# Optimization experiments

Hardware: AMD Instinct MI355X
Metric: run time of the kernel (lower is better)

## Reference

```python
import jax, jax.numpy as jnp
import numpy as np

B, T, C, H = 4, 2048, 1024, 16
HS = C // H  # head_size = 64
EPS = 1e-5


def setup_inputs() -> dict:
    key = jax.random.key(0)
    ks = jax.random.split(key, 16)
    s = 0.02
    inp = {
        "x": jax.random.normal(ks[0], (B, T, C), jnp.float32),
        # custom LayerNorm buffers (gamma=ones, beta=zeros in source)
        "ln1_g": jnp.ones((C,), jnp.float32),
        "ln1_b": jnp.zeros((C,), jnp.float32),
        "ln2_g": jnp.ones((C,), jnp.float32),
        "ln2_b": jnp.zeros((C,), jnp.float32),
        # per-head Q/K/V linears, stacked over heads: [H, C, HS]
        "Wq": jax.random.normal(ks[1], (H, C, HS), jnp.float32) * s,
        "bq": jax.random.normal(ks[2], (H, HS), jnp.float32) * s,
        "Wk": jax.random.normal(ks[3], (H, C, HS), jnp.float32) * s,
        "bk": jax.random.normal(ks[4], (H, HS), jnp.float32) * s,
        "Wv": jax.random.normal(ks[5], (H, C, HS), jnp.float32) * s,
        "bv": jax.random.normal(ks[6], (H, HS), jnp.float32) * s,
        # output projection [C, C]
        "Wo": jax.random.normal(ks[7], (C, C), jnp.float32) * s,
        "bo": jax.random.normal(ks[8], (C,), jnp.float32) * s,
        # FFN: C -> 4C -> C
        "W1": jax.random.normal(ks[9], (C, 4 * C), jnp.float32) * s,
        "b1": jax.random.normal(ks[10], (4 * C,), jnp.float32) * s,
        "W2": jax.random.normal(ks[11], (4 * C, C), jnp.float32) * s,
        "b2": jax.random.normal(ks[12], (C,), jnp.float32) * s,
    }
    return inp


def _layernorm_time_axis(x, g, b):
    # Faithful to source: normalizes over axis=1 (time), unbiased variance (ddof=1).
    m = jnp.mean(x, axis=1, keepdims=True)
    v = jnp.var(x, axis=1, keepdims=True, ddof=1)
    return g * (x - m) / jnp.sqrt(v + EPS) + b


def reference(x, ln1_g, ln1_b, ln2_g, ln2_b, Wq, bq, Wk, bk, Wv, bv, Wo, bo, W1, b1, W2, b2):
    Bc, Tc, Cc = x.shape
    h = _layernorm_time_axis(x, ln1_g, ln1_b)
    # per-head projections: [B, H, T, HS]
    q = jnp.einsum('btc,hcd->bhtd', h, Wq) + bq[None, :, None, :]
    k = jnp.einsum('btc,hcd->bhtd', h, Wk) + bk[None, :, None, :]
    v = jnp.einsum('btc,hcd->bhtd', h, Wv) + bv[None, :, None, :]
    # scores scaled by C**-0.5 (full embed dim, as in source)
    wei = jnp.einsum('bhtd,bhsd->bhts', q, k) * (Cc ** -0.5)
    causal = jnp.tril(jnp.ones((Tc, Tc), bool))
    wei = jnp.where(causal[None, None], wei, -jnp.inf)
    wei = jax.nn.softmax(wei, axis=-1)
    att = jnp.einsum('bhts,bhsd->bhtd', wei, v)
    # concat heads -> [B, T, C], then projection
    att = att.transpose(0, 2, 1, 3).reshape(Bc, Tc, Cc)
    x = x + att @ Wo + bo
    # FFN on ln2
    h2 = _layernorm_time_axis(x, ln2_g, ln2_b)
    ff = jax.nn.relu(h2 @ W1 + b1) @ W2 + b2
    return x + ff
```

## Files before the change

kernel.cpp:

```cpp
#include <hip/hip_runtime.h>

#define B_   4
#define T_   2048
#define C_   1024
#define H_   16
#define HS_  64
#define BT_  (B_*T_)
#define EPS_ 1e-5f

typedef unsigned short u16;
typedef unsigned int   u32;
typedef __attribute__((ext_vector_type(8))) __bf16 bf16x8;
typedef __attribute__((ext_vector_type(4))) float  f32x4;
typedef __attribute__((ext_vector_type(8))) u16    u16x8;
typedef __attribute__((ext_vector_type(4))) u16    u16x4;
typedef __attribute__((ext_vector_type(4))) u32    u32x4;

__device__ __forceinline__ u16 f2bf(float f) {
  unsigned x = __builtin_bit_cast(unsigned, f);
  x += 0x7fffu + ((x >> 16) & 1u);
  return (u16)(x >> 16);
}
__device__ __forceinline__ float bf2f(u16 v) {
  return __builtin_bit_cast(float, (u32)v << 16);
}

__device__ __forceinline__ float fast_exp2(float x) {
  float y;
  asm("v_exp_f32 %0, %1" : "=v"(y) : "v"(x));
  return y;
}
__device__ __forceinline__ float fast_rcp(float x) {
  float y;
  asm("v_rcp_f32 %0, %1" : "=v"(y) : "v"(x));
  return y;
}

#define GLD_LDS16(src, dst) \
  __builtin_amdgcn_global_load_lds((__attribute__((address_space(1))) void*)(src), \
                                   (__attribute__((address_space(3))) void*)(dst), 16, 0, 0)

__global__ __launch_bounds__(256) void ln_partial_bf(const u16* __restrict__ x,
                                                     float* __restrict__ ps,
                                                     float* __restrict__ psq) {
  int col = blockIdx.x * 256 + threadIdx.x;
  int b = col >> 10, c = col & (C_ - 1);
  int t0 = blockIdx.y * (T_ / 16);
  const u16* p = x + (size_t)b * T_ * C_ + (size_t)t0 * C_ + c;
  float s = 0.f, sq = 0.f;
  #pragma unroll 4
  for (int i = 0; i < T_ / 16; ++i) { float v = bf2f(p[(size_t)i * C_]); s += v; sq += v * v; }
  ps [blockIdx.y * (B_ * C_) + col] = s;
  psq[blockIdx.y * (B_ * C_) + col] = sq;
}

__global__ __launch_bounds__(256) void ln_final(const float* __restrict__ ps,
                                                const float* __restrict__ psq,
                                                float* __restrict__ mean,
                                                float* __restrict__ rstd) {
  int col = blockIdx.x * 256 + threadIdx.x;
  float s = 0.f, sq = 0.f;
  #pragma unroll
  for (int i = 0; i < 16; ++i) { s += ps[i * (B_ * C_) + col]; sq += psq[i * (B_ * C_) + col]; }
  float m = s * (1.f / T_);
  float var = (sq - (float)T_ * m * m) * (1.f / (T_ - 1));
  mean[col] = m;
  rstd[col] = rsqrtf(var + EPS_);
}

__global__ __launch_bounds__(256) void ln_norm(const float* __restrict__ x,
                                               const float* __restrict__ mean,
                                               const float* __restrict__ rstd,
                                               const float* __restrict__ gam,
                                               const float* __restrict__ bet,
                                               u16* __restrict__ out) {
  size_t i = ((size_t)blockIdx.x * 256 + threadIdx.x) * 4;
  int c  = (int)(i & (C_ - 1));
  int b  = (int)(i >> 21);
  int bc = (b << 10) + c;
  float4 v = *(const float4*)(x + i);
  float vv[4] = {v.x, v.y, v.z, v.w};
  u16x4 o;
  #pragma unroll
  for (int j = 0; j < 4; ++j)
    o[j] = f2bf(gam[c + j] * (vv[j] - mean[bc + j]) * rstd[bc + j] + bet[c + j]);
  *(u16x4*)(out + i) = o;
}

__global__ __launch_bounds__(256) void ln_norm_bf(const u16* __restrict__ x,
                                                  const float* __restrict__ mean,
                                                  const float* __restrict__ rstd,
                                                  const float* __restrict__ gam,
                                                  const float* __restrict__ bet,
                                                  u16* __restrict__ out) {
  size_t i = ((size_t)blockIdx.x * 256 + threadIdx.x) * 4;
  int c  = (int)(i & (C_ - 1));
  int b  = (int)(i >> 21);
  int bc = (b << 10) + c;
  u16x4 v = *(const u16x4*)(x + i);
  u16x4 o;
  #pragma unroll
  for (int j = 0; j < 4; ++j)
    o[j] = f2bf(gam[c + j] * (bf2f(v[j]) - mean[bc + j]) * rstd[bc + j] + bet[c + j]);
  *(u16x4*)(out + i) = o;
}

__global__ __launch_bounds__(256) void pack_all(
    const float* __restrict__ Wq, const float* __restrict__ Wk,
    const float* __restrict__ Wv, const float* __restrict__ Wo,
    const float* __restrict__ W1, const float* __restrict__ W2,
    const float* __restrict__ bq, const float* __restrict__ bk,
    const float* __restrict__ bv, const float* __restrict__ x,
    u16* __restrict__ wqkvT, u16* __restrict__ woT,
    u16* __restrict__ w1T,   u16* __restrict__ w2T,
    float* __restrict__ bqkv,
    float* __restrict__ ps,  float* __restrict__ psq) {
  __shared__ float tile[32][33];
  const int bid = blockIdx.x;
  const int tid = threadIdx.x;

  if (bid >= 12300) {
    const int rel = bid - 12300;
    const int bx = rel & 15, by = rel >> 4;
    int col = bx * 256 + tid;
    int b = col >> 10, c = col & (C_ - 1);
    int t0 = by * (T_ / 16);
    const float* p = x + (size_t)b * T_ * C_ + (size_t)t0 * C_ + c;
    float s = 0.f, sq = 0.f;
    #pragma unroll 4
    for (int i = 0; i < T_ / 16; ++i) { float v = p[(size_t)i * C_]; s += v; sq += v * v; }
    ps [by * (B_ * C_) + col] = s;
    psq[by * (B_ * C_) + col] = sq;
    return;
  }
  if (bid >= 12288) {
    int i = (bid - 12288) * 256 + tid;
    float v = (i < 1024) ? bq[i] : (i < 2048 ? bk[i - 1024] : bv[i - 2048]);
    bqkv[i] = v;
    return;
  }

  const float* I; u16* Ou; int cols_in, ld_out, bx, by;
  if (bid < 3072) {
    const int z = bid >> 6, t6 = bid & 63;
    bx = t6 & 1; by = t6 >> 1;
    const int wsel = z >> 4, head = z & 15;
    I  = (wsel == 0 ? Wq : (wsel == 1 ? Wk : Wv)) + (size_t)head * (C_ * 64);
    Ou = wqkvT + (size_t)wsel * 1024 * 1024 + (size_t)head * 64 * 1024;
    cols_in = 64; ld_out = 1024;
  } else if (bid < 4096) {
    const int rel = bid - 3072;
    bx = rel & 31; by = rel >> 5;
    I = Wo; Ou = woT; cols_in = 1024; ld_out = 1024;
  } else if (bid < 8192) {
    const int rel = bid - 4096;
    bx = rel & 127; by = rel >> 7;
    I = W1; Ou = w1T; cols_in = 4096; ld_out = 1024;
  } else {
    const int rel = bid - 8192;
    bx = rel & 31; by = rel >> 5;
    I = W2; Ou = w2T; cols_in = 1024; ld_out = 4096;
  }

  const int r0 = by << 5, c0 = bx << 5;
  const int tx = tid & 31, ty = tid >> 5;
  #pragma unroll
  for (int rr = 0; rr < 32; rr += 8)
    tile[ty + rr][tx] = I[(size_t)(r0 + ty + rr) * cols_in + c0 + tx];
  __syncthreads();
  #pragma unroll
  for (int rr = 0; rr < 32; rr += 8)
    Ou[(size_t)(c0 + ty + rr) * ld_out + r0 + tx] = f2bf(tile[tx][ty + rr]);
}

__global__ __launch_bounds__(256) void v_transpose(const u16* __restrict__ qkv,
                                                   u16* __restrict__ Vt) {
  __shared__ u16 tile[32][33];
  int bh = blockIdx.z; int b = bh >> 4, h = bh & 15;
  int t0 = blockIdx.x << 5, hs0 = blockIdx.y << 5;
  int tx = threadIdx.x & 31, ty = threadIdx.x >> 5;
  const u16* src = qkv + (size_t)(b * T_ + t0) * 3072 + 2048 + h * 64 + hs0;
  #pragma unroll
  for (int rr = 0; rr < 32; rr += 8)
    tile[ty + rr][tx] = src[(size_t)(ty + rr) * 3072 + tx];
  __syncthreads();
  u16* dst = Vt + ((size_t)bh * 64 + hs0) * T_ + t0;
  #pragma unroll
  for (int rr = 0; rr < 32; rr += 8)
    dst[(size_t)(ty + rr) * T_ + tx] = tile[tx][ty + rr];
}

template<int BN, int RELU, int QSCALE>
__global__ __launch_bounds__(256, 2)
void gemm_128t(const u16* __restrict__ A,
               const u16* __restrict__ Bt,
               const float* __restrict__ bias,
               u16* __restrict__ outp,
               int M, int N, int K) {
  constexpr int BK  = 32;
  constexpr int CHA = 2;
  constexpr int CHB = BN / 64;
  constexpr int NF  = BN / 32;

  __shared__ u16 sA[3][128 * BK];
  __shared__ u16 sB[3][BN * BK];

  const int tid = threadIdx.x;
  const int wave = tid >> 6, lane = tid & 63;
  const int g = lane >> 4, r16 = lane & 15;

  const int nbx = N / BN;
  const int nwg = gridDim.x;
  const int bid = blockIdx.x;
  const int swz = ((bid & 7) * (nwg >> 3)) + (bid >> 3);
  const int bx = swz % nbx, by = swz / nbx;
  const int row0 = by << 7, col0 = bx * BN;

  const u16* aS[CHA];
  const u16* bS[CHB];
  #pragma unroll
  for (int j = 0; j < CHA; ++j) {
    const int ci = tid + 256 * j, row = ci >> 2, cc = ci & 3;
    aS[j] = A + (size_t)(row0 + row) * K + ((cc ^ ((row >> 1) & 3)) * 8);
  }
  #pragma unroll
  for (int j = 0; j < CHB; ++j) {
    const int ci = tid + 256 * j, row = ci >> 2, cc = ci & 3;
    bS[j] = Bt + (size_t)(col0 + row) * K + ((cc ^ ((row >> 1) & 3)) * 8);
  }
  const int ldsOff = wave * 512;

  auto stage = [&](int t, int buf) {
    const int ko = t * BK;
    #pragma unroll
    for (int j = 0; j < CHA; ++j)
      GLD_LDS16(aS[j] + ko, &sA[buf][ldsOff + j * 2048]);
    #pragma unroll
    for (int j = 0; j < CHB; ++j)
      GLD_LDS16(bS[j] + ko, &sB[buf][ldsOff + j * 2048]);
  };

  auto wait_stage1 = [&]() {
    if constexpr (CHB == 4) asm volatile("s_waitcnt vmcnt(6)" ::: "memory");
    else                    asm volatile("s_waitcnt vmcnt(5)" ::: "memory");
  };

  const int wrow = (wave >> 1) * 64;
  const int wcol = (wave & 1) * (BN >> 1);
  f32x4 acc[4][NF] = {};

  const int NT = K / BK;

  stage(0, 0); stage(1, 1);
  wait_stage1();
  __builtin_amdgcn_s_barrier();
  __builtin_amdgcn_sched_barrier(0);

  for (int t = 0; t < NT; ++t) {
    const u16* As = sA[t % 3];
    const u16* Bs = sB[t % 3];
    bf16x8 af[4], bf[NF];
    #pragma unroll
    for (int m = 0; m < 4; ++m) {
      const int lr = wrow + m * 16 + r16;
      af[m] = *(const bf16x8*)&As[lr * 32 + ((g ^ ((lr >> 1) & 3)) * 8)];
    }
    #pragma unroll
    for (int n = 0; n < NF; ++n) {
      const int lr = wcol + n * 16 + r16;
      bf[n] = *(const bf16x8*)&Bs[lr * 32 + ((g ^ ((lr >> 1) & 3)) * 8)];
    }
    if (t + 2 < NT) stage(t + 2, (t + 2) % 3);

    __builtin_amdgcn_s_setprio(1);
    #pragma unroll
    for (int m = 0; m < 4; ++m)
      #pragma unroll
      for (int n = 0; n < NF; ++n)
        acc[m][n] = __builtin_amdgcn_mfma_f32_16x16x32_bf16(af[m], bf[n], acc[m][n], 0, 0, 0);
    __builtin_amdgcn_s_setprio(0);

    if (t + 1 < NT) {
      if (t + 2 < NT) wait_stage1();
      else            asm volatile("s_waitcnt vmcnt(0)" ::: "memory");
      __builtin_amdgcn_s_barrier();
      __builtin_amdgcn_sched_barrier(0);
    }
  }

  #pragma unroll
  for (int m = 0; m < 4; ++m) {
    #pragma unroll
    for (int n = 0; n < NF; ++n) {
      const int col = col0 + wcol + n * 16 + r16;
      const float bv = bias[col];
      const float sc = (QSCALE && col < 1024) ? 0.04508422003f : 1.f;
      const int rowb = row0 + wrow + m * 16 + g * 4;
      #pragma unroll
      for (int r = 0; r < 4; ++r) {
        float v = acc[m][n][r] + bv;
        if (RELU) v = fmaxf(v, 0.f);
        if (QSCALE) v *= sc;
        outp[(size_t)(rowb + r) * N + col] = f2bf(v);
      }
    }
  }
}

template<int RELU, int RAW, int QSCALE>
__global__ __launch_bounds__(512, 2)
void gemm_256(const u16* __restrict__ A,
              const u16* __restrict__ Bt,
              const float* __restrict__ bias,
              const u16* __restrict__ resb,
              void* __restrict__ outp,
              void* __restrict__ outp_b,
              int M, int N, int K) {
  constexpr int BK = 32;
  __shared__ u16 sA[4][256 * BK];
  __shared__ u16 sB[4][256 * BK];

  const int tid = threadIdx.x;
  const int wave = tid >> 6, lane = tid & 63;
  const int g = lane >> 4, r16 = lane & 15;

  const int nbx = N >> 8;
  const int nwg = gridDim.x;
  const int bid = blockIdx.x;
  const int swz = ((bid & 7) * (nwg >> 3)) + (bid >> 3);
  const int bx = swz % nbx, by = swz / nbx;
  const int row0 = by << 8, col0 = bx << 8;

  const int kspan = RAW ? (K >> 1) : K;
  const int kbase = RAW ? ((int)blockIdx.y * kspan) : 0;

  const u16* aS[2];
  const u16* bS[2];
  #pragma unroll
  for (int j = 0; j < 2; ++j) {
    const int ci = tid + 512 * j, row = ci >> 2, cc = ci & 3;
    aS[j] = A  + (size_t)(row0 + row) * K + ((cc ^ ((row >> 1) & 3)) * 8) + kbase;
    bS[j] = Bt + (size_t)(col0 + row) * K + ((cc ^ ((row >> 1) & 3)) * 8) + kbase;
  }
  const int ldsOff = wave * 512;

  auto stage = [&](int t, int buf) {
    const int ko = t * BK;
    #pragma unroll
    for (int j = 0; j < 2; ++j)
      GLD_LDS16(aS[j] + ko, &sA[buf][ldsOff + j * 4096]);
    #pragma unroll
    for (int j = 0; j < 2; ++j)
      GLD_LDS16(bS[j] + ko, &sB[buf][ldsOff + j * 4096]);
  };

  const int wrow = (wave >> 2) * 128;
  const int wcol = (wave & 3) * 64;
  f32x4 acc[8][4] = {};

  const int NT = kspan / BK;

  stage(0, 0); stage(1, 1);
  asm volatile("s_waitcnt vmcnt(4)" ::: "memory");
  __builtin_amdgcn_s_barrier();
  __builtin_amdgcn_sched_barrier(0);

  for (int t = 0; t < NT; ++t) {
    const u16* As = sA[t & 3];
    const u16* Bs = sB[t & 3];
    bf16x8 af[8], bf[4];
    #pragma unroll
    for (int m = 0; m < 8; ++m) {
      const int lr = wrow + m * 16 + r16;
      af[m] = *(const bf16x8*)&As[lr * 32 + ((g ^ ((lr >> 1) & 3)) * 8)];
    }
    #pragma unroll
    for (int n = 0; n < 4; ++n) {
      const int lr = wcol + n * 16 + r16;
      bf[n] = *(const bf16x8*)&Bs[lr * 32 + ((g ^ ((lr >> 1) & 3)) * 8)];
    }
    if (t + 2 < NT) stage(t + 2, (t + 2) & 3);

    __builtin_amdgcn_s_setprio(1);
    #pragma unroll
    for (int m = 0; m < 8; ++m)
      #pragma unroll
      for (int n = 0; n < 4; ++n)
        acc[m][n] = __builtin_amdgcn_mfma_f32_16x16x32_bf16(af[m], bf[n], acc[m][n], 0, 0, 0);
    __builtin_amdgcn_s_setprio(0);

    if (t + 1 < NT) {
      if (t + 2 < NT) asm volatile("s_waitcnt vmcnt(4)" ::: "memory");
      else            asm volatile("s_waitcnt vmcnt(0)" ::: "memory");
      __builtin_amdgcn_s_barrier();
      __builtin_amdgcn_sched_barrier(0);
    }
  }

  if constexpr (RAW) {
    if (blockIdx.y) {
      float* po = (float*)outp_b;
      #pragma unroll
      for (int m = 0; m < 8; ++m) {
        #pragma unroll
        for (int n = 0; n < 4; ++n) {
          const int col = col0 + wcol + n * 16 + r16;
          const float bv = bias[col];
          const int rowb = row0 + wrow + m * 16 + g * 4;
          #pragma unroll
          for (int r = 0; r < 4; ++r) {
            const size_t idx = (size_t)(rowb + r) * N + col;
            po[idx] = acc[m][n][r] + bv + bf2f(resb[idx]);
          }
        }
      }
    } else {
      u16* po = (u16*)outp;
      #pragma unroll
      for (int m = 0; m < 8; ++m) {
        #pragma unroll
        for (int n = 0; n < 4; ++n) {
          const int col = col0 + wcol + n * 16 + r16;
          const int rowb = row0 + wrow + m * 16 + g * 4;
          #pragma unroll
          for (int r = 0; r < 4; ++r)
            po[(size_t)(rowb + r) * N + col] = f2bf(acc[m][n][r]);
        }
      }
    }
  } else {
    u16* po = (u16*)outp;
    #pragma unroll
    for (int m = 0; m < 8; ++m) {
      #pragma unroll
      for (int n = 0; n < 4; ++n) {
        const int col = col0 + wcol + n * 16 + r16;
        const float bv = bias[col];
        const float sc = (QSCALE && col < 1024) ? 0.04508422003f : 1.f;
        const int rowb = row0 + wrow + m * 16 + g * 4;
        #pragma unroll
        for (int r = 0; r < 4; ++r) {
          float v = acc[m][n][r] + bv;
          if (RELU) v = fmaxf(v, 0.f);
          if (QSCALE) v *= sc;
          po[(size_t)(rowb + r) * N + col] = f2bf(v);
        }
      }
    }
  }
}

__global__ __launch_bounds__(256) void ffn2_reduce(const u16* __restrict__ pA,
                                                   float* __restrict__ out) {
  size_t i = ((size_t)blockIdx.x * 256 + threadIdx.x) * 4;
  u16x4 a = *(const u16x4*)(pA + i);
  float4 o = *(const float4*)(out + i);
  float4 v;
  v.x = o.x + bf2f(a[0]);
  v.y = o.y + bf2f(a[1]);
  v.z = o.z + bf2f(a[2]);
  v.w = o.w + bf2f(a[3]);
  *(float4*)(out + i) = v;
}

template<int BM, int BN, int THREADS, int OUT_F32, int RELU, int RES>
__global__ __launch_bounds__(THREADS, 3)
void gemm_pipe(const u16* __restrict__ A,
               const u16* __restrict__ Bt,
               const float* __restrict__ bias,
               const float* __restrict__ res,
               void* __restrict__ outp,
               int M, int N, int K) {
  constexpr int BK  = 32;
  constexpr int CHA = (BM * 4) / THREADS;
  constexpr int CHB = (BN * 4) / THREADS;
  constexpr int CH  = CHA + CHB;

  __shared__ u16 sA[3][BM * BK];
  __shared__ u16 sB[3][BN * BK];

  const int tid = threadIdx.x;
  const int wave = tid >> 6, lane = tid & 63;
  const int g = lane >> 4, r16 = lane & 15;

  const int nbx = N / BN;
  const int nwg = gridDim.x;
  const int bid = blockIdx.x;
  const int swz = ((bid & 7) * (nwg >> 3)) + (bid >> 3);
  const int bx = swz % nbx, by = swz / nbx;
  const int row0 = by * BM, col0 = bx * BN;

  const u16* aS[CHA];
  const u16* bS[CHB];
  #pragma unroll
  for (int j = 0; j < CHA; ++j) {
    const int ci = tid + THREADS * j, row = ci >> 2, cc = ci & 3;
    aS[j] = A + (size_t)(row0 + row) * K + ((cc ^ ((row >> 1) & 3)) * 8);
  }
  #pragma unroll
  for (int j = 0; j < CHB; ++j) {
    const int ci = tid + THREADS * j, row = ci >> 2, cc = ci & 3;
    bS[j] = Bt + (size_t)(col0 + row) * K + ((cc ^ ((row >> 1) & 3)) * 8);
  }
  const int ldsOff = wave * 512;

  auto stage = [&](int t, int buf) {
    const int ko = t * BK;
    #pragma unroll
    for (int j = 0; j < CHA; ++j)
      GLD_LDS16(aS[j] + ko, &sA[buf][ldsOff + j * (THREADS * 8)]);
    #pragma unroll
    for (int j = 0; j < CHB; ++j)
      GLD_LDS16(bS[j] + ko, &sB[buf][ldsOff + j * (THREADS * 8)]);
  };

  const int wrow = (wave >> 1) * 64;
  const int wcol = (wave & 1) * 64;
  f32x4 acc[4][4] = {};

  const int NT = K / BK;

  stage(0, 0); stage(1, 1);
  if constexpr (CH == 3) asm volatile("s_waitcnt vmcnt(3)" ::: "memory");
  else                   asm volatile("s_waitcnt vmcnt(4)" ::: "memory");
  __builtin_amdgcn_s_barrier();
  __builtin_amdgcn_sched_barrier(0);

  for (int t = 0; t < NT; ++t) {
    if (t + 2 < NT) stage(t + 2, (t + 2) % 3);
    const u16* As = sA[t % 3];
    const u16* Bs = sB[t % 3];
    bf16x8 af[4], bf[4];
    #pragma unroll
    for (int m = 0; m < 4; ++m) {
      const int lr = wrow + m * 16 + r16;
      af[m] = *(const bf16x8*)&As[lr * 32 + ((g ^ ((lr >> 1) & 3)) * 8)];
    }
    #pragma unroll
    for (int n = 0; n < 4; ++n) {
      const int lr = wcol + n * 16 + r16;
      bf[n] = *(const bf16x8*)&Bs[lr * 32 + ((g ^ ((lr >> 1) & 3)) * 8)];
    }
    __builtin_amdgcn_s_setprio(1);
    #pragma unroll
    for (int m = 0; m < 4; ++m)
      #pragma unroll
      for (int n = 0; n < 4; ++n)
        acc[m][n] = __builtin_amdgcn_mfma_f32_16x16x32_bf16(af[m], bf[n], acc[m][n], 0, 0, 0);
    __builtin_amdgcn_s_setprio(0);

    if (t + 1 < NT) {
      if (t + 2 < NT) {
        if constexpr (CH == 3) asm volatile("s_waitcnt vmcnt(3)" ::: "memory");
        else                   asm volatile("s_waitcnt vmcnt(4)" ::: "memory");
      } else {
        asm volatile("s_waitcnt vmcnt(0)" ::: "memory");
      }
      __builtin_amdgcn_s_barrier();
      __builtin_amdgcn_sched_barrier(0);
    }
  }

  #pragma unroll
  for (int m = 0; m < 4; ++m) {
    #pragma unroll
    for (int n = 0; n < 4; ++n) {
      const int col = col0 + wcol + n * 16 + r16;
      const float bv = bias[col];
      const int rowb = row0 + wrow + m * 16 + g * 4;
      #pragma unroll
      for (int r = 0; r < 4; ++r) {
        const size_t idx = (size_t)(rowb + r) * N + col;
        float v = acc[m][n][r] + bv;
        if (RES)  v += res[idx];
        if (RELU) v = fmaxf(v, 0.f);
        if (OUT_F32) ((float*)outp)[idx] = v;
        else         ((u16*)outp)[idx]   = f2bf(v);
      }
    }
  }
}

__global__ __launch_bounds__(256, 2) void attn_fwd(const u16* __restrict__ qkv,
                                                   const u16* __restrict__ Vt,
                                                   u16* __restrict__ O) {
  __shared__ u16 sK[2][64 * 64];
  __shared__ u16 sV[2][64 * 64];

  const int orig = blockIdx.x;
  const int work = ((orig & 7) << 6) + (orig >> 3);
  const int i = work & 7;
  const int h = (work >> 3) & 15;
  const int b = work >> 7;
  const int qA = i << 7, qB = (15 - i) << 7;
  const int nA = 2 * i + 2, nB = 32 - 2 * i;

  const int tid = threadIdx.x, wave = tid >> 6, lane = tid & 63;
  const int g = lane >> 4, r16 = lane & 15;

  const size_t base = (size_t)b * T_ * 3072 + h * 64;
  const u16* Qp = qkv + base;
  const u16* Kp = qkv + base + 1024;
  const u16* VtP = Vt + (size_t)(b * 16 + h) * 64 * T_;

  const int rowL = lane >> 3;
  const int colL = 8 * ((lane & 7) ^ rowL);
  const u16* kSrc = Kp  + (size_t)(wave * 16 + rowL) * 3072 + colL;
  const u16* vSrc = VtP + (size_t)(wave * 16 + rowL) * T_   + colL;
  u16* kDst0 = &sK[0][(wave * 16 + 0) * 64];
  u16* kDst8 = &sK[0][(wave * 16 + 8) * 64];
  u16* vDst0 = &sV[0][(wave * 16 + 0) * 64];
  u16* vDst8 = &sV[0][(wave * 16 + 8) * 64];

  const int ck0 = (( 0 + g * 16) ^ ((r16 & 7) << 4)) >> 1;
  const int ck1 = ((64 + g * 16) ^ ((r16 & 7) << 4)) >> 1;

  bf16x8 qfA[2][2], qfB[2][2];
  #pragma unroll
  for (int qp = 0; qp < 2; ++qp)
    #pragma unroll
    for (int kc = 0; kc < 2; ++kc) {
      qfA[qp][kc] = *(const bf16x8*)(Qp + (size_t)(qA + wave * 32 + qp * 16 + r16) * 3072 + kc * 32 + g * 8);
      qfB[qp][kc] = *(const bf16x8*)(Qp + (size_t)(qB + wave * 32 + qp * 16 + r16) * 3072 + kc * 32 + g * 8);
    }

  f32x4 accA[2][4] = {}, accB[2][4] = {};
  f32x4 lA[2] = {}, lB[2] = {};
  int qaA[2], qaB[2];
  #pragma unroll
  for (int qp = 0; qp < 2; ++qp) {
    qaA[qp] = qA + wave * 32 + qp * 16 + r16;
    qaB[qp] = qB + wave * 32 + qp * 16 + r16;
  }

  const u32 one2 = 0x3F803F80u;
  const u32x4 onesv = {one2, one2, one2, one2};
  const bf16x8 ONES = __builtin_bit_cast(bf16x8, onesv);

  int sbuf = 0;
  auto stageAdv = [&]() {
    const int o = sbuf * 4096;
    GLD_LDS16(kSrc,            kDst0 + o);
    GLD_LDS16(kSrc + 8 * 3072, kDst8 + o);
    GLD_LDS16(vSrc,            vDst0 + o);
    GLD_LDS16(vSrc + 8 * T_,   vDst8 + o);
    kSrc += 64 * 3072;
    vSrc += 64;
    sbuf ^= 1;
  };

  auto qkt = [&](const bf16x8* kf0, const bf16x8* kf1, const bf16x8* qf, f32x4* s) {
    __builtin_amdgcn_s_setprio(1);
    #pragma unroll
    for (int ni = 0; ni < 4; ++ni) {
      f32x4 t = {};
      t = __builtin_amdgcn_mfma_f32_16x16x32_bf16(kf0[ni], qf[0], t, 0, 0, 0);
      t = __builtin_amdgcn_mfma_f32_16x16x32_bf16(kf1[ni], qf[1], t, 0, 0, 0);
      s[ni] = t;
    }
    __builtin_amdgcn_s_setprio(0);
  };

  auto softmax_pack = [&](f32x4* s, bool diag, int q_abs, int kv0, bf16x8* pa) {
    if (diag) {
      #pragma unroll
      for (int ni = 0; ni < 4; ++ni)
        #pragma unroll
        for (int r = 0; r < 4; ++r) {
          const int kv_abs = kv0 + ni * 16 + g * 4 + r;
          if (kv_abs > q_abs) s[ni][r] = -3e38f;
        }
    }
    #pragma unroll
    for (int ni = 0; ni < 4; ++ni)
      #pragma unroll
      for (int r = 0; r < 4; ++r)
        s[ni][r] = fast_exp2(s[ni][r]);

    u32 pk[4][2];
    #pragma unroll
    for (int ni = 0; ni < 4; ++ni)
      #pragma unroll
      for (int h2 = 0; h2 < 2; ++h2)
        asm("v_cvt_pk_bf16_f32 %0, %1, %2"
            : "=v"(pk[ni][h2]) : "v"(s[ni][2 * h2]), "v"(s[ni][2 * h2 + 1]));

    u32 pa32[2][4];
    #pragma unroll
    for (int kc = 0; kc < 2; ++kc)
      #pragma unroll
      for (int h2 = 0; h2 < 2; ++h2) {
        u32 a = pk[2 * kc][h2], bq_ = pk[2 * kc + 1][h2];
        asm("v_permlane32_swap_b32 %0, %1" : "+v"(a), "+v"(bq_));
        asm("v_permlane16_swap_b32 %0, %1" : "+v"(a), "+v"(bq_));
        pa32[kc][h2] = a;
        pa32[kc][2 + h2] = bq_;
      }
    #pragma unroll
    for (int kc = 0; kc < 2; ++kc) {
      u32x4 tmp = {pa32[kc][0], pa32[kc][1], pa32[kc][2], pa32[kc][3]};
      pa[kc] = __builtin_bit_cast(bf16x8, tmp);
    }
  };

  stageAdv();
  asm volatile("s_waitcnt vmcnt(0)" ::: "memory");
  __builtin_amdgcn_s_barrier();
  __builtin_amdgcn_sched_barrier(0);

  int cbuf = 0;
  for (int t = 0; t < nB; ++t) {
    if (t + 1 < nB) stageAdv();
    const u16* Kb = sK[cbuf];
    const u16* Vb = sV[cbuf];
    const int kv0 = t << 6;
    const bool actA = (t < nA);
    const bool mB = (t + 2 >= nB);
    const bool mA = (t + 2 >= nA);

    bf16x8 kf0[4], kf1[4], vf0[4], vf1[4];
    #pragma unroll
    for (int ni = 0; ni < 4; ++ni) {
      kf0[ni] = *(const bf16x8*)&Kb[(ni * 16 + r16) * 64 + ck0];
      kf1[ni] = *(const bf16x8*)&Kb[(ni * 16 + r16) * 64 + ck1];
      vf0[ni] = *(const bf16x8*)&Vb[(ni * 16 + r16) * 64 + ck0];
      vf1[ni] = *(const bf16x8*)&Vb[(ni * 16 + r16) * 64 + ck1];
    }

    #pragma unroll
    for (int qp = 0; qp < 2; ++qp) {
      f32x4 s[4];
      bf16x8 pa[2];
      qkt(kf0, kf1, qfB[qp], s);
      softmax_pack(s, mB, qaB[qp], kv0, pa);
      __builtin_amdgcn_s_setprio(1);
      lB[qp] = __builtin_amdgcn_mfma_f32_16x16x32_bf16(pa[0], ONES, lB[qp], 0, 0, 0);
      lB[qp] = __builtin_amdgcn_mfma_f32_16x16x32_bf16(pa[1], ONES, lB[qp], 0, 0, 0);
      #pragma unroll
      for (int hsb = 0; hsb < 4; ++hsb) {
        accB[qp][hsb] = __builtin_amdgcn_mfma_f32_16x16x32_bf16(pa[0], vf0[hsb], accB[qp][hsb], 0, 0, 0);
        accB[qp][hsb] = __builtin_amdgcn_mfma_f32_16x16x32_bf16(pa[1], vf1[hsb], accB[qp][hsb], 0, 0, 0);
      }
      __builtin_amdgcn_s_setprio(0);
    }

    if (actA) {
      #pragma unroll
      for (int qp = 0; qp < 2; ++qp) {
        f32x4 s[4];
        bf16x8 pa[2];
        qkt(kf0, kf1, qfA[qp], s);
        softmax_pack(s, mA, qaA[qp], kv0, pa);
        __builtin_amdgcn_s_setprio(1);
        lA[qp] = __builtin_amdgcn_mfma_f32_16x16x32_bf16(pa[0], ONES, lA[qp], 0, 0, 0);
        lA[qp] = __builtin_amdgcn_mfma_f32_16x16x32_bf16(pa[1], ONES, lA[qp], 0, 0, 0);
        #pragma unroll
        for (int hsb = 0; hsb < 4; ++hsb) {
          accA[qp][hsb] = __builtin_amdgcn_mfma_f32_16x16x32_bf16(pa[0], vf0[hsb], accA[qp][hsb], 0, 0, 0);
          accA[qp][hsb] = __builtin_amdgcn_mfma_f32_16x16x32_bf16(pa[1], vf1[hsb], accA[qp][hsb], 0, 0, 0);
        }
        __builtin_amdgcn_s_setprio(0);
      }
    }

    if (t + 1 < nB) {
      asm volatile("s_waitcnt vmcnt(0)" ::: "memory");
      __builtin_amdgcn_s_barrier();
      __builtin_amdgcn_sched_barrier(0);
    }
    cbuf ^= 1;
  }

  #pragma unroll
  for (int qp = 0; qp < 2; ++qp) {
    float rlA[4], rlB[4];
    #pragma unroll
    for (int r = 0; r < 4; ++r) {
      rlA[r] = fast_rcp(lA[qp][r]);
      rlB[r] = fast_rcp(lB[qp][r]);
    }
    #pragma unroll
    for (int hsb = 0; hsb < 4; ++hsb)
      #pragma unroll
      for (int r = 0; r < 4; ++r) {
        const size_t rowA = (size_t)b * T_ + qA + wave * 32 + qp * 16 + g * 4 + r;
        const size_t rowB = (size_t)b * T_ + qB + wave * 32 + qp * 16 + g * 4 + r;
        O[rowA * C_ + h * 64 + hsb * 16 + r16] = f2bf(accA[qp][hsb][r] * rlA[r]);
        O[rowB * C_ + h * 64 + hsb * 16 + r16] = f2bf(accB[qp][hsb][r] * rlB[r]);
      }
  }
}

extern "C" void kernel_launch(void* const* d_in, const int* in_sizes, int n_in,
                              void* d_out, int out_size, void* d_ws, size_t ws_size,
                              hipStream_t stream) {
  const float* x    = (const float*)d_in[0];
  const float* ln1g = (const float*)d_in[1];
  const float* ln1b = (const float*)d_in[2];
  const float* ln2g = (const float*)d_in[3];
  const float* ln2b = (const float*)d_in[4];
  const float* Wq   = (const float*)d_in[5];
  const float* bq   = (const float*)d_in[6];
  const float* Wk   = (const float*)d_in[7];
  const float* bk   = (const float*)d_in[8];
  const float* Wv   = (const float*)d_in[9];
  const float* bv   = (const float*)d_in[10];
  const float* Wo   = (const float*)d_in[11];
  const float* bo   = (const float*)d_in[12];
  const float* W1   = (const float*)d_in[13];
  const float* b1   = (const float*)d_in[14];
  const float* W2   = (const float*)d_in[15];
  const float* b2   = (const float*)d_in[16];

  char* w = (char*)d_ws;
  float* ps    = (float*)(w + 0);
  float* psq   = (float*)(w + 262144);
  float* mean  = (float*)(w + 524288);
  float* rstd  = (float*)(w + 540672);
  float* bqkv  = (float*)(w + 557056);
  u16*   h     = (u16*)  (w + 573440);
  u16*   wqkvT = (u16*)  (w + 17350656);
  u16*   woT   = (u16*)  (w + 23642112);
  u16*   w1T   = (u16*)  (w + 25739264);
  u16*   w2T   = (u16*)  (w + 34127872);
  u16*   x1b   = (u16*)  (w + 42516480);
  u16*   Vt    = (u16*)  (w + 59293696);
  u16*   qkv   = (u16*)  (w + 76070912);
  u16*   Oo    = (u16*)  (w + 126402560);
  u16*   u     = qkv;
  u16*   pA    = (u16*)  (w + 573440);

  pack_all<<<12556, 256, 0, stream>>>(Wq, Wk, Wv, Wo, W1, W2, bq, bk, bv, x,
                                      wqkvT, woT, w1T, w2T, bqkv, ps, psq);

  ln_final<<<16, 256, 0, stream>>>(ps, psq, mean, rstd);
  ln_norm<<<8192, 256, 0, stream>>>(x, mean, rstd, ln1g, ln1b, h);

  gemm_128t<192, 0, 1><<<1024, 256, 0, stream>>>(h, wqkvT, bqkv, qkv, BT_, 3072, 1024);

  v_transpose<<<dim3(T_ / 32, 2, B_ * H_), 256, 0, stream>>>(qkv, Vt);

  attn_fwd<<<512, 256, 0, stream>>>(qkv, Vt, Oo);

  gemm_pipe<128, 128, 256, 0, 0, 1><<<512, 256, 0, stream>>>(Oo, woT, bo, x, x1b, BT_, 1024, 1024);

  ln_partial_bf<<<dim3(16, 16), 256, 0, stream>>>(x1b, ps, psq);
  ln_final<<<16, 256, 0, stream>>>(ps, psq, mean, rstd);
  ln_norm_bf<<<8192, 256, 0, stream>>>(x1b, mean, rstd, ln2g, ln2b, h);

  gemm_256<1, 0, 0><<<512, 512, 0, stream>>>(h, w1T, b1, nullptr, u, nullptr, BT_, 4096, 1024);
  gemm_256<0, 1, 0><<<dim3(128, 2), 512, 0, stream>>>(u, w2T, b2, x1b, pA, d_out, BT_, 1024, 4096);
  ffn2_reduce<<<8192, 256, 0, stream>>>(pA, (float*)d_out);
}
```

Baseline: 361.7 us.

## Fuse V transpose into QKV GEMM epilogue and triple-buffer attention K/V

The QKV projection epilogue now also writes V columns directly in transposed [b,h,hs,t] layout, removing the separate v_transpose launch and its reread of qkv. The attention kernel moves from double to triple buffering of K/V tiles in LDS, prefetching two tiles ahead with partial vmcnt waits to hide global-load latency. The trade-offs are strided scattered 2-byte stores in the GEMM epilogue and extra LDS per block, which could lower occupancy.

```diff
diff --git a/kernel.cpp b/kernel.cpp
--- a/kernel.cpp
+++ b/kernel.cpp
@@ -173,29 +173,13 @@
     Ou[(size_t)(c0 + ty + rr) * ld_out + r0 + tx] = f2bf(tile[tx][ty + rr]);
 }
 
-__global__ __launch_bounds__(256) void v_transpose(const u16* __restrict__ qkv,
-                                                   u16* __restrict__ Vt) {
-  __shared__ u16 tile[32][33];
-  int bh = blockIdx.z; int b = bh >> 4, h = bh & 15;
-  int t0 = blockIdx.x << 5, hs0 = blockIdx.y << 5;
-  int tx = threadIdx.x & 31, ty = threadIdx.x >> 5;
-  const u16* src = qkv + (size_t)(b * T_ + t0) * 3072 + 2048 + h * 64 + hs0;
-  #pragma unroll
-  for (int rr = 0; rr < 32; rr += 8)
-    tile[ty + rr][tx] = src[(size_t)(ty + rr) * 3072 + tx];
-  __syncthreads();
-  u16* dst = Vt + ((size_t)bh * 64 + hs0) * T_ + t0;
-  #pragma unroll
-  for (int rr = 0; rr < 32; rr += 8)
-    dst[(size_t)(ty + rr) * T_ + tx] = tile[tx][ty + rr];
-}
-
-template<int BN, int RELU, int QSCALE>
+template<int BN, int RELU, int QSCALE, int VT>
 __global__ __launch_bounds__(256, 2)
 void gemm_128t(const u16* __restrict__ A,
                const u16* __restrict__ Bt,
                const float* __restrict__ bias,
                u16* __restrict__ outp,
+               u16* __restrict__ vtout,
                int M, int N, int K) {
   constexpr int BK  = 32;
   constexpr int CHA = 2;
@@ -301,7 +285,16 @@
         float v = acc[m][n][r] + bv;
         if (RELU) v = fmaxf(v, 0.f);
         if (QSCALE) v *= sc;
-        outp[(size_t)(rowb + r) * N + col] = f2bf(v);
+        const u16 o = f2bf(v);
+        outp[(size_t)(rowb + r) * N + col] = o;
+        if constexpr (VT) {
+          if (col >= 2048) {
+            const int bb = rowb >> 11;
+            const int tt = (rowb + r) & 2047;
+            const int hh = (col - 2048) >> 6, hs = (col - 2048) & 63;
+            vtout[((size_t)(bb * 16 + hh) * 64 + hs) * T_ + tt] = o;
+          }
+        }
       }
     }
   }
@@ -584,8 +577,8 @@
 __global__ __launch_bounds__(256, 2) void attn_fwd(const u16* __restrict__ qkv,
                                                    const u16* __restrict__ Vt,
                                                    u16* __restrict__ O) {
-  __shared__ u16 sK[2][64 * 64];
-  __shared__ u16 sV[2][64 * 64];
+  __shared__ u16 sK[3][64 * 64];
+  __shared__ u16 sV[3][64 * 64];
 
   const int orig = blockIdx.x;
   const int work = ((orig & 7) << 6) + (orig >> 3);
@@ -646,7 +639,7 @@
     GLD_LDS16(vSrc + 8 * T_,   vDst8 + o);
     kSrc += 64 * 3072;
     vSrc += 64;
-    sbuf ^= 1;
+    sbuf = (sbuf == 2) ? 0 : sbuf + 1;
   };
 
   auto qkt = [&](const bf16x8* kf0, const bf16x8* kf1, const bf16x8* qf, f32x4* s) {
@@ -704,13 +697,14 @@
   };
 
   stageAdv();
-  asm volatile("s_waitcnt vmcnt(0)" ::: "memory");
+  stageAdv();
+  asm volatile("s_waitcnt vmcnt(4)" ::: "memory");
   __builtin_amdgcn_s_barrier();
   __builtin_amdgcn_sched_barrier(0);
 
   int cbuf = 0;
   for (int t = 0; t < nB; ++t) {
-    if (t + 1 < nB) stageAdv();
+    if (t + 2 < nB) stageAdv();
     const u16* Kb = sK[cbuf];
     const u16* Vb = sV[cbuf];
     const int kv0 = t << 6;
@@ -764,11 +758,12 @@
     }
 
     if (t + 1 < nB) {
-      asm volatile("s_waitcnt vmcnt(0)" ::: "memory");
+      if (t + 2 < nB) asm volatile("s_waitcnt vmcnt(4)" ::: "memory");
+      else            asm volatile("s_waitcnt vmcnt(0)" ::: "memory");
       __builtin_amdgcn_s_barrier();
       __builtin_amdgcn_sched_barrier(0);
     }
-    cbuf ^= 1;
+    cbuf = (cbuf == 2) ? 0 : cbuf + 1;
   }
 
   #pragma unroll
@@ -836,9 +831,7 @@
   ln_final<<<16, 256, 0, stream>>>(ps, psq, mean, rstd);
   ln_norm<<<8192, 256, 0, stream>>>(x, mean, rstd, ln1g, ln1b, h);
 
-  gemm_128t<192, 0, 1><<<1024, 256, 0, stream>>>(h, wqkvT, bqkv, qkv, BT_, 3072, 1024);
-
-  v_transpose<<<dim3(T_ / 32, 2, B_ * H_), 256, 0, stream>>>(qkv, Vt);
+  gemm_128t<192, 0, 1, 1><<<1024, 256, 0, stream>>>(h, wqkvT, bqkv, qkv, Vt, BT_, 3072, 1024);
 
   attn_fwd<<<512, 256, 0, stream>>>(qkv, Vt, Oo);
 
```

New measurement: 399.6 us. 1.1x slower.
